# Optimization experiments

Hardware: AMD Instinct MI355X
Metric: run time of the kernel (lower is better)

The kernel has to match this reference:

```python
import jax, jax.numpy as jnp
import numpy as np

B, N, L, C, H = 4, 4096, 1024, 1024, 16
D = C // H  # head_dim = 64
SCALE = 1.0 / np.sqrt(D)


def setup_inputs() -> dict:
    key = jax.random.key(0)
    ks = jax.random.split(key, 5)
    return {
        "x": jax.random.normal(ks[0], (B, N, C), dtype=jnp.float32),
        "query": jax.random.normal(ks[1], (B, L, C), dtype=jnp.float32),
        "Wq": jax.random.normal(ks[2], (C, C), dtype=jnp.float32) * 0.02,
        "Wkv": jax.random.normal(ks[3], (2 * C, C), dtype=jnp.float32) * 0.02,
        "Wproj": jax.random.normal(ks[4], (C, C), dtype=jnp.float32) * 0.02,
        "bproj": jnp.zeros((C,), dtype=jnp.float32),
    }


def reference(x, query, Wq, Wkv, Wproj, bproj):
    # q projection: [B,L,C] -> [B,H,L,D]
    q = (query @ Wq.T).reshape(B, L, H, D).transpose(0, 2, 1, 3)
    # kv projection: [B,N,2C] -> k,v each [B,H,N,D]
    kv = (x @ Wkv.T).reshape(B, N, 2, H, D).transpose(2, 0, 3, 1, 4)
    k, v = kv[0], kv[1]
    # unfused SDPA: explicit [B,H,L,N] score matrix (faithful to source)
    attn = jnp.einsum('bhld,bhnd->bhln', q, k) * SCALE
    attn = jax.nn.softmax(attn, axis=-1)
    out = jnp.einsum('bhln,bhnd->bhld', attn, v)  # [B,H,L,D]
    out = out.transpose(0, 2, 1, 3).reshape(B, L, C)
    return out @ Wproj.T + bproj
```

## Files before the change

kernel.cpp:

```cpp
#include <hip/hip_runtime.h>
#include <hip/hip_bf16.h>

typedef __attribute__((ext_vector_type(8))) short short8;
typedef __attribute__((ext_vector_type(4))) float floatx4;

#if __has_builtin(__builtin_amdgcn_exp2f)
#define EXP2(x) __builtin_amdgcn_exp2f(x)
#else
#define EXP2(x) exp2f(x)
#endif

#define BAR() __builtin_amdgcn_s_barrier()
#define FENCE() asm volatile("" ::: "memory")
#define WAIT_LGKM0() asm volatile("s_waitcnt lgkmcnt(0)" ::: "memory")
#define WAIT_VM(n) asm volatile("s_waitcnt vmcnt(" #n ")" ::: "memory")

__device__ __forceinline__ short f2bf(float f) {
  __hip_bfloat16 h = __float2bfloat16(f);
  return *reinterpret_cast<const short*>(&h);
}

__device__ __forceinline__ short8 cvt_f32x8_bf16(const float* __restrict__ p) {
  float4 a = *reinterpret_cast<const float4*>(p);
  float4 b = *reinterpret_cast<const float4*>(p + 4);
  short8 r;
  r[0] = f2bf(a.x); r[1] = f2bf(a.y); r[2] = f2bf(a.z); r[3] = f2bf(a.w);
  r[4] = f2bf(b.x); r[5] = f2bf(b.y); r[6] = f2bf(b.z); r[7] = f2bf(b.w);
  return r;
}

typedef const __attribute__((address_space(1))) void* gptr1;
typedef __attribute__((address_space(3))) void* lptr3;
__device__ __forceinline__ void gl_lds16(const void* g, void* l) {
  __builtin_amdgcn_global_load_lds((gptr1)g, (lptr3)l, 16, 0, 0);
}

__global__ __launch_bounds__(256)
void f32_to_bf16(const float* __restrict__ in, short* __restrict__ out, int n8) {
  int i = blockIdx.x * blockDim.x + threadIdx.x;
  if (i < n8) {
    short8 v = cvt_f32x8_bf16(in + (size_t)i * 8);
    *reinterpret_cast<short8*>(out + (size_t)i * 8) = v;
  }
}

__global__ __launch_bounds__(256)
void conv_weights(const float* __restrict__ Wkv, const float* __restrict__ Wq,
                  const float* __restrict__ Wproj, short* __restrict__ wkvb,
                  short* __restrict__ wqb, short* __restrict__ wprojb) {
  const float* src; short* dst; int off;
  int i = blockIdx.x * 256 + threadIdx.x;
  if (blockIdx.x < 1024)      { src = Wkv;   dst = wkvb;   off = i; }
  else if (blockIdx.x < 1536) { src = Wq;    dst = wqb;    off = i - 1024 * 256; }
  else                        { src = Wproj; dst = wprojb; off = i - 1536 * 256; }
  short8 v = cvt_f32x8_bf16(src + (size_t)off * 8);
  *reinterpret_cast<short8*>(dst + (size_t)off * 8) = v;
}

__global__ __launch_bounds__(512, 2)
void gemm256_kv(const short* __restrict__ A, const short* __restrict__ B,
                short* __restrict__ k_out, short* __restrict__ vt,
                int M, int N, int K)
{
  __shared__ __align__(16) short lds[2][2][2][128 * 64];

  const int tid  = threadIdx.x;
  const int lane = tid & 63;
  const int w    = tid >> 6;
  const int wm   = w >> 2;
  const int wn   = w & 3;
  const int cl   = lane & 15;
  const int hi   = lane >> 4;
  const int srl  = lane >> 3;
  const int gch8 = (((lane & 7) ^ srl) << 3);

  const int ntile = N >> 8;
  int bid = blockIdx.x;
  { int cpx = gridDim.x >> 3; bid = (bid & 7) * cpx + (bid >> 3); }
  const int tm = bid / ntile, tn = bid % ntile;
  const int m0 = tm << 8, n0 = tn << 8;
  const int NT = K >> 6;

  auto stageA = [&](int par, int slot, int ktX) {
    #pragma unroll
    for (int j = 0; j < 2; ++j) {
      const int sr = (w << 4) + (j << 3) + srl;
      const int tr = ((sr >> 6) << 7) + (slot << 6) + (sr & 63);
      gl_lds16(A + (size_t)(m0 + tr) * K + ktX + gch8,
               (void*)&lds[par][0][slot][((w << 4) + (j << 3)) * 64]);
    }
  };
  auto stageB = [&](int par, int slot, int ktX) {
    #pragma unroll
    for (int j = 0; j < 2; ++j) {
      const int sr = (w << 4) + (j << 3) + srl;
      const int tr = ((sr >> 5) << 6) + (slot << 5) + (sr & 31);
      gl_lds16(B + (size_t)(n0 + tr) * K + ktX + gch8,
               (void*)&lds[par][1][slot][((w << 4) + (j << 3)) * 64]);
    }
  };

  const floatx4 fzero = {0.f, 0.f, 0.f, 0.f};
  floatx4 acc[8][4];
  #pragma unroll
  for (int m = 0; m < 8; ++m)
    #pragma unroll
    for (int n = 0; n < 4; ++n)
      acc[m][n] = fzero;

  short8 af[4][2], b0[2][2], b1[2][2];

  auto readA = [&](int par, int slot) {
    #pragma unroll
    for (int m = 0; m < 4; ++m)
      #pragma unroll
      for (int ks = 0; ks < 2; ++ks) {
        const int sr = (wm << 6) + (m << 4) + cl;
        const int cpos = ((((ks << 2) + hi) ^ (sr & 7)) << 3);
        af[m][ks] = *reinterpret_cast<const short8*>(&lds[par][0][slot][sr * 64 + cpos]);
      }
  };
  auto readB = [&](int par, int slot, short8 (&bf)[2][2]) {
    #pragma unroll
    for (int n = 0; n < 2; ++n)
      #pragma unroll
      for (int ks = 0; ks < 2; ++ks) {
        const int sr = (wn << 5) + (n << 4) + cl;
        const int cpos = ((((ks << 2) + hi) ^ (sr & 7)) << 3);
        bf[n][ks] = *reinterpret_cast<const short8*>(&lds[par][1][slot][sr * 64 + cpos]);
      }
  };

  #define QUAD(BF, MH, NH)                                                     \
    __builtin_amdgcn_s_setprio(1);                                             \
    _Pragma("unroll")                                                          \
    for (int ks = 0; ks < 2; ++ks)                                             \
      _Pragma("unroll")                                                        \
      for (int m = 0; m < 4; ++m)                                              \
        _Pragma("unroll")                                                      \
        for (int n = 0; n < 2; ++n)                                            \
          acc[(MH)*4 + m][(NH)*2 + n] = __builtin_amdgcn_mfma_f32_16x16x32_bf16( \
              af[m][ks], BF[n][ks], acc[(MH)*4 + m][(NH)*2 + n], 0, 0, 0);     \
    __builtin_amdgcn_s_setprio(0);

  stageA(0, 0, 0); stageB(0, 0, 0); stageB(0, 1, 0); stageA(0, 1, 0);
  stageA(1, 0, 64); stageB(1, 0, 64); stageB(1, 1, 64);
  WAIT_VM(6); BAR(); FENCE();

  for (int t = 0; t < NT; ++t) {
    const int p  = t & 1;
    const int pn = p ^ 1;
    int t1 = t + 1; if (t1 >= NT) t1 -= NT;
    int t2 = t + 2; if (t2 >= NT) t2 -= NT;
    const int kt1 = t1 << 6;
    const int kt2 = t2 << 6;

    readA(p, 0); readB(p, 0, b0);
    stageA(pn, 1, kt1);
    BAR(); WAIT_LGKM0();
    QUAD(b0, 0, 0);
    BAR(); FENCE();

    readB(p, 1, b1);
    stageA(p, 0, kt2);
    BAR(); WAIT_LGKM0();
    QUAD(b1, 0, 1);
    BAR(); FENCE();

    readA(p, 1);
    stageB(p, 0, kt2);
    BAR(); WAIT_LGKM0();
    QUAD(b0, 1, 0);
    BAR(); FENCE();

    stageB(p, 1, kt2);
    WAIT_VM(6);
    BAR(); WAIT_LGKM0();
    QUAD(b1, 1, 1);
    BAR(); FENCE();
  }
  WAIT_VM(0);

  const int rq = hi << 2;
  #pragma unroll
  for (int Mi = 0; Mi < 8; ++Mi) {
    #pragma unroll
    for (int Nn = 0; Nn < 4; ++Nn) {
      const int grow = m0 + wm * 128 + Mi * 16 + rq;
      const int gcol = n0 + wn * 64 + Nn * 16 + cl;
      if (gcol < 1024) {
        #pragma unroll
        for (int i = 0; i < 4; ++i)
          k_out[(size_t)(grow + i) * 1024 + gcol] = f2bf(acc[Mi][Nn][i]);
      } else {
        const int d  = gcol - 1024;
        const int bb = grow >> 12;
        const int nn = grow & 4095;
        size_t base = ((size_t)(bb * 16 + (d >> 6)) * 64 + (d & 63)) * 4096 + nn;
        short4 pk;
        pk.x = f2bf(acc[Mi][Nn][0]); pk.y = f2bf(acc[Mi][Nn][1]);
        pk.z = f2bf(acc[Mi][Nn][2]); pk.w = f2bf(acc[Mi][Nn][3]);
        *reinterpret_cast<short4*>(&vt[base]) = pk;
      }
    }
  }
}

template<int MODE>
__global__ __launch_bounds__(256, 4)
void gemm64(const short* __restrict__ A, const short* __restrict__ B,
            void* __restrict__ O0, const float* __restrict__ bias,
            int M, int N, int K, float oscale)
{
  __shared__ __align__(16) short As[64 * 64];
  __shared__ __align__(16) short Bs[64 * 64];

  const int tid  = threadIdx.x;
  const int lane = tid & 63;
  const int w    = tid >> 6;
  const int ntile = N >> 6;
  int bid = blockIdx.x;
  { int cpx = gridDim.x >> 3; bid = (bid & 7) * cpx + (bid >> 3); }
  const int tm = bid / ntile;
  const int tn = bid % ntile;
  const int m0 = tm << 6, n0 = tn << 6;
  const int wr = (w >> 1) << 5;
  const int wc = (w & 1) << 5;
  const int cl = lane & 15;
  const int hi = lane >> 4;
  const int srow = lane >> 3;
  const int scol = (lane & 7) << 3;

  const floatx4 fzero = {0.f, 0.f, 0.f, 0.f};
  floatx4 acc[2][2];
  #pragma unroll
  for (int m = 0; m < 2; ++m)
    #pragma unroll
    for (int n = 0; n < 2; ++n)
      acc[m][n] = fzero;

  for (int kt = 0; kt < K; kt += 64) {
    #pragma unroll
    for (int i = 0; i < 2; ++i) {
      const int chunk = (w << 1) + i;
      const int row   = (chunk << 3) + srow;
      gl_lds16(A + (size_t)(m0 + row) * K + kt + scol, &As[chunk * 512]);
      gl_lds16(B + (size_t)(n0 + row) * K + kt + scol, &Bs[chunk * 512]);
    }
    __syncthreads();

    #pragma unroll
    for (int ks = 0; ks < 2; ++ks) {
      short8 af[2], bfr[2];
      #pragma unroll
      for (int m = 0; m < 2; ++m)
        af[m] = *reinterpret_cast<const short8*>(
            &As[(wr + m * 16 + cl) * 64 + ks * 32 + (hi << 3)]);
      #pragma unroll
      for (int n = 0; n < 2; ++n)
        bfr[n] = *reinterpret_cast<const short8*>(
            &Bs[(wc + n * 16 + cl) * 64 + ks * 32 + (hi << 3)]);
      #pragma unroll
      for (int m = 0; m < 2; ++m)
        #pragma unroll
        for (int n = 0; n < 2; ++n)
          acc[m][n] = __builtin_amdgcn_mfma_f32_16x16x32_bf16(af[m], bfr[n], acc[m][n], 0, 0, 0);
    }
    __syncthreads();
  }

  const int rq = hi << 2;
  #pragma unroll
  for (int m = 0; m < 2; ++m) {
    #pragma unroll
    for (int n = 0; n < 2; ++n) {
      const int grow = m0 + wr + m * 16 + rq;
      const int gcol = n0 + wc + n * 16 + cl;
      if (MODE == 0) {
        short* o = (short*)O0;
        #pragma unroll
        for (int i = 0; i < 4; ++i)
          o[(size_t)(grow + i) * N + gcol] = f2bf(acc[m][n][i] * oscale);
      } else {
        float* o = (float*)O0;
        const float bv = bias[gcol];
        #pragma unroll
        for (int i = 0; i < 4; ++i)
          o[(size_t)(grow + i) * N + gcol] = acc[m][n][i] + bv;
      }
    }
  }
}

__global__ __launch_bounds__(256, 2)
void attn_fwd(const short* __restrict__ q_ws, const short* __restrict__ k_ws,
              const short* __restrict__ vt_ws, short* __restrict__ ao_ws)
{
  __shared__ __align__(16) short Ks[2][64 * 64];
  __shared__ __align__(16) short Vts[2][64 * 64];
  __shared__ __align__(16) short Pl[2][4][32 * 64];

  const int tid  = threadIdx.x;
  const int lane = tid & 63;
  const int w    = tid >> 6;
  const int i    = blockIdx.x;
  const int bh   = (i & 7) * 8 + (i >> 6);
  const int qt   = (i >> 3) & 7;
  const int b  = bh >> 4;
  const int h  = bh & 15;
  const int q0 = qt * 128 + w * 32;
  const int cl = lane & 15;
  const int hi = lane >> 4;
  const int rq = hi << 2;
  const int key7 = cl & 7;

  short8 qf[2][2];
  #pragma unroll
  for (int tt = 0; tt < 2; ++tt)
    #pragma unroll
    for (int ks = 0; ks < 2; ++ks) {
      size_t idx = (size_t)(b * 1024 + q0 + tt * 16 + cl) * 1024
                 + h * 64 + ks * 32 + (hi << 3);
      qf[tt][ks] = *reinterpret_cast<const short8*>(&q_ws[idx]);
    }

  int koff[2];
  #pragma unroll
  for (int ks = 0; ks < 2; ++ks)
    koff[ks] = cl * 64 + ((((ks << 2) + hi) ^ key7) << 3);
  const int pwc   = hi >> 1;
  const int pwoff = (hi & 1) << 2;
  int pwch[4];
  #pragma unroll
  for (int n = 0; n < 4; ++n)
    pwch[n] = ((((n << 1) + pwc) ^ key7) << 3) + pwoff + cl * 64;

  const floatx4 fzero = {0.f, 0.f, 0.f, 0.f};
  floatx4 o[2][4];
  floatx4 ol[2];
  floatx4 s[4][2];
  short8 vones;
  #pragma unroll
  for (int j = 0; j < 8; ++j) vones[j] = (short)0x3F80;
  #pragma unroll
  for (int tt = 0; tt < 2; ++tt) {
    ol[tt] = fzero;
    #pragma unroll
    for (int nd = 0; nd < 4; ++nd) o[tt][nd] = fzero;
  }

  const int c0    = w << 1;
  const int srow8 = lane >> 3;
  const int gch8  = (((lane & 7) ^ srow8) << 3);
  const short* kbase = k_ws + (size_t)(b * 4096 + (c0 << 3) + srow8) * 1024 + h * 64 + gch8;
  const short* vbase = vt_ws + ((size_t)bh * 64 + (c0 << 3) + srow8) * 4096 + gch8;

  auto stage = [&](int buf, int kv0) {
    gl_lds16(kbase + (size_t)kv0 * 1024,          (void*)&Ks[buf][c0 * 512]);
    gl_lds16(kbase + (size_t)kv0 * 1024 + 8192,   (void*)&Ks[buf][(c0 + 1) * 512]);
    gl_lds16(vbase + kv0,                          (void*)&Vts[buf][c0 * 512]);
    gl_lds16(vbase + kv0 + 8 * 4096,               (void*)&Vts[buf][(c0 + 1) * 512]);
  };

  auto qk = [&](const short* kb) {
    short8 kf[2][4];
    #pragma unroll
    for (int ks = 0; ks < 2; ++ks)
      #pragma unroll
      for (int n = 0; n < 4; ++n)
        kf[ks][n] = *reinterpret_cast<const short8*>(kb + koff[ks] + n * 1024);
    #pragma unroll
    for (int n = 0; n < 4; ++n)
      #pragma unroll
      for (int tt = 0; tt < 2; ++tt)
        s[n][tt] = __builtin_amdgcn_mfma_f32_16x16x32_bf16(
            kf[1][n], qf[tt][1],
            __builtin_amdgcn_mfma_f32_16x16x32_bf16(kf[0][n], qf[tt][0], fzero, 0, 0, 0),
            0, 0, 0);
  };
  auto pv = [&](const short* plb, const short* vb) {
    #pragma unroll
    for (int ks = 0; ks < 2; ++ks) {
      short8 pa[2], vf[4];
      #pragma unroll
      for (int tt = 0; tt < 2; ++tt)
        pa[tt] = *reinterpret_cast<const short8*>(plb + koff[ks] + tt * 1024);
      #pragma unroll
      for (int nd = 0; nd < 4; ++nd)
        vf[nd] = *reinterpret_cast<const short8*>(vb + koff[ks] + nd * 1024);
      #pragma unroll
      for (int tt = 0; tt < 2; ++tt) {
        ol[tt] = __builtin_amdgcn_mfma_f32_16x16x32_bf16(pa[tt], vones, ol[tt], 0, 0, 0);
        #pragma unroll
        for (int nd = 0; nd < 4; ++nd)
          o[tt][nd] = __builtin_amdgcn_mfma_f32_16x16x32_bf16(pa[tt], vf[nd], o[tt][nd], 0, 0, 0);
      }
    }
  };
  auto smax = [&](short* plw) {
    #pragma unroll
    for (int tt = 0; tt < 2; ++tt)
      #pragma unroll
      for (int n = 0; n < 4; ++n) {
        short4 pk;
        #pragma unroll
        for (int ii = 0; ii < 4; ++ii)
          pk[ii] = f2bf(EXP2(s[n][tt][ii]));
        *reinterpret_cast<short4*>(plw + tt * 1024 + pwch[n]) = pk;
      }
  };

  stage(0, 0);
  WAIT_VM(0); BAR(); FENCE();
  qk(&Ks[0][0]);
  stage(1, 64);
  smax(&Pl[0][w][0]);
  int pb = 0;

  for (int t = 0; t < 63; ++t) {
    const int cur = t & 1;
    WAIT_VM(0); BAR(); FENCE();
    __builtin_amdgcn_s_setprio(1);
    qk(&Ks[cur ^ 1][0]);
    pv(&Pl[pb][w][0], &Vts[cur][0]);
    __builtin_amdgcn_s_setprio(0);
    FENCE(); BAR();
    stage(cur, ((t + 2) & 63) << 6);
    smax(&Pl[pb ^ 1][w][0]);
    pb ^= 1;
  }
  __builtin_amdgcn_s_setprio(1);
  pv(&Pl[pb][w][0], &Vts[1][0]);
  __builtin_amdgcn_s_setprio(0);
  WAIT_VM(0);

  #pragma unroll
  for (int m = 0; m < 2; ++m) {
    float inv[4];
    #pragma unroll
    for (int ii = 0; ii < 4; ++ii)
      inv[ii] = 1.f / ol[m][ii];
    #pragma unroll
    for (int nd = 0; nd < 4; ++nd)
      #pragma unroll
      for (int ii = 0; ii < 4; ++ii) {
        size_t idx = (size_t)(b * 1024 + q0 + m * 16 + rq + ii) * 1024
                   + h * 64 + nd * 16 + cl;
        ao_ws[idx] = f2bf(o[m][nd][ii] * inv[ii]);
      }
  }
}

extern "C" void kernel_launch(void* const* d_in, const int* in_sizes, int n_in,
                              void* d_out, int out_size, void* d_ws, size_t ws_size,
                              hipStream_t stream)
{
  const float* x     = (const float*)d_in[0];
  const float* query = (const float*)d_in[1];
  const float* Wq    = (const float*)d_in[2];
  const float* Wkv   = (const float*)d_in[3];
  const float* Wproj = (const float*)d_in[4];
  const float* bproj = (const float*)d_in[5];
  float* out = (float*)d_out;

  const float QSCALE = 0.18033688011112042f;

  char* ws = (char*)d_ws;
  short* k_ws   = (short*)(ws);
  short* vt_ws  = (short*)(ws + (32ull << 20));
  short* xb     = (short*)(ws + (64ull << 20));
  short* qb     = (short*)(ws + (64ull << 20));
  short* q_ws   = (short*)(ws + (72ull << 20));
  short* ao_ws  = (short*)(ws + (80ull << 20));
  short* wkvb   = (short*)(ws + (96ull << 20));
  short* wqb    = (short*)(ws + (100ull << 20));
  short* wprojb = (short*)(ws + (102ull << 20));

  conv_weights<<<dim3(2048), 256, 0, stream>>>(Wkv, Wq, Wproj, wkvb, wqb, wprojb);
  f32_to_bf16<<<dim3(8192), 256, 0, stream>>>(x, xb, (16384 * 1024) / 8);

  gemm256_kv<<<dim3(512), 512, 0, stream>>>(xb, wkvb, k_ws, vt_ws,
                                            16384, 2048, 1024);
  f32_to_bf16<<<dim3(2048), 256, 0, stream>>>(query, qb, (4096 * 1024) / 8);
  gemm64<0><<<dim3(1024), 256, 0, stream>>>(qb, wqb, q_ws, nullptr,
                                            4096, 1024, 1024, QSCALE);
  attn_fwd<<<dim3(512), 256, 0, stream>>>(q_ws, k_ws, vt_ws, ao_ws);
  gemm64<2><<<dim3(1024), 256, 0, stream>>>(ao_ws, wprojb, out, bproj,
                                            4096, 1024, 1024, 1.0f);
}
```

Measured before the change: 209.8 us.

## Merge conversion kernels, fuse query cast into Q GEMM, single-buffer P in attention

Folds the x and weight fp32-to-bf16 conversions into one launch, and drops the separate query conversion by having the Q-projection GEMM read fp32 and convert while staging into LDS. The KV GEMM stops issuing wrapped-around prefetch loads on its last two iterations. The attention kernel single-buffers its P tile, adds an LDS wait before the softmax write, and raises the occupancy hint from 2 to 3 blocks per CU. The aim is fewer launches and less redundant memory traffic. The costs are synchronous register-path loads in the Q GEMM instead of direct-to-LDS copies, and less overlap in attention.

```diff
diff --git a/kernel.cpp b/kernel.cpp
--- a/kernel.cpp
+++ b/kernel.cpp
@@ -36,25 +36,19 @@
 }
 
 __global__ __launch_bounds__(256)
-void f32_to_bf16(const float* __restrict__ in, short* __restrict__ out, int n8) {
-  int i = blockIdx.x * blockDim.x + threadIdx.x;
-  if (i < n8) {
-    short8 v = cvt_f32x8_bf16(in + (size_t)i * 8);
-    *reinterpret_cast<short8*>(out + (size_t)i * 8) = v;
-  }
-}
-
-__global__ __launch_bounds__(256)
-void conv_weights(const float* __restrict__ Wkv, const float* __restrict__ Wq,
-                  const float* __restrict__ Wproj, short* __restrict__ wkvb,
-                  short* __restrict__ wqb, short* __restrict__ wprojb) {
-  const float* src; short* dst; int off;
-  int i = blockIdx.x * 256 + threadIdx.x;
-  if (blockIdx.x < 1024)      { src = Wkv;   dst = wkvb;   off = i; }
-  else if (blockIdx.x < 1536) { src = Wq;    dst = wqb;    off = i - 1024 * 256; }
-  else                        { src = Wproj; dst = wprojb; off = i - 1536 * 256; }
-  short8 v = cvt_f32x8_bf16(src + (size_t)off * 8);
-  *reinterpret_cast<short8*>(dst + (size_t)off * 8) = v;
+void conv_all(const float* __restrict__ x, const float* __restrict__ Wkv,
+              const float* __restrict__ Wq, const float* __restrict__ Wproj,
+              short* __restrict__ xb, short* __restrict__ wkvb,
+              short* __restrict__ wqb, short* __restrict__ wprojb) {
+  const float* src; short* dst; size_t off;
+  int bi = blockIdx.x;
+  int i = bi * 256 + threadIdx.x;
+  if (bi < 8192)      { src = x;     dst = xb;     off = i; }
+  else if (bi < 9216) { src = Wkv;   dst = wkvb;   off = i - 8192 * 256; }
+  else if (bi < 9728) { src = Wq;    dst = wqb;    off = i - 9216 * 256; }
+  else                { src = Wproj; dst = wprojb; off = i - 9728 * 256; }
+  short8 v = cvt_f32x8_bf16(src + off * 8);
+  *reinterpret_cast<short8*>(dst + off * 8) = v;
 }
 
 __global__ __launch_bounds__(512, 2)
@@ -150,36 +144,35 @@
   for (int t = 0; t < NT; ++t) {
     const int p  = t & 1;
     const int pn = p ^ 1;
-    int t1 = t + 1; if (t1 >= NT) t1 -= NT;
-    int t2 = t + 2; if (t2 >= NT) t2 -= NT;
+    const int t1 = t + 1;
+    const int t2 = t + 2;
     const int kt1 = t1 << 6;
     const int kt2 = t2 << 6;
 
     readA(p, 0); readB(p, 0, b0);
-    stageA(pn, 1, kt1);
+    if (t1 < NT) stageA(pn, 1, kt1);
     BAR(); WAIT_LGKM0();
     QUAD(b0, 0, 0);
     BAR(); FENCE();
 
     readB(p, 1, b1);
-    stageA(p, 0, kt2);
+    if (t2 < NT) stageA(p, 0, kt2);
     BAR(); WAIT_LGKM0();
     QUAD(b1, 0, 1);
     BAR(); FENCE();
 
     readA(p, 1);
-    stageB(p, 0, kt2);
+    if (t2 < NT) stageB(p, 0, kt2);
     BAR(); WAIT_LGKM0();
     QUAD(b0, 1, 0);
     BAR(); FENCE();
 
-    stageB(p, 1, kt2);
-    WAIT_VM(6);
+    if (t2 < NT) { stageB(p, 1, kt2); WAIT_VM(6); }
+    else         { WAIT_VM(0); }
     BAR(); WAIT_LGKM0();
     QUAD(b1, 1, 1);
     BAR(); FENCE();
   }
-  WAIT_VM(0);
 
   const int rq = hi << 2;
   #pragma unroll
@@ -206,9 +199,9 @@
   }
 }
 
-template<int MODE>
+template<int MODE, bool AFP32>
 __global__ __launch_bounds__(256, 4)
-void gemm64(const short* __restrict__ A, const short* __restrict__ B,
+void gemm64(const void* __restrict__ Ap, const short* __restrict__ B,
             void* __restrict__ O0, const float* __restrict__ bias,
             int M, int N, int K, float oscale)
 {
@@ -240,11 +233,29 @@
       acc[m][n] = fzero;
 
   for (int kt = 0; kt < K; kt += 64) {
+    if (AFP32) {
+      const float* A = (const float*)Ap;
+      #pragma unroll
+      for (int sgm = 0; sgm < 2; ++sgm) {
+        const int seg = tid + sgm * 256;
+        const int row = seg >> 3;
+        const int c8  = (seg & 7) << 3;
+        short8 v = cvt_f32x8_bf16(A + (size_t)(m0 + row) * K + kt + c8);
+        *reinterpret_cast<short8*>(&As[row * 64 + c8]) = v;
+      }
+    } else {
+      const short* A = (const short*)Ap;
+      #pragma unroll
+      for (int i = 0; i < 2; ++i) {
+        const int chunk = (w << 1) + i;
+        const int row   = (chunk << 3) + srow;
+        gl_lds16(A + (size_t)(m0 + row) * K + kt + scol, &As[chunk * 512]);
+      }
+    }
     #pragma unroll
     for (int i = 0; i < 2; ++i) {
       const int chunk = (w << 1) + i;
       const int row   = (chunk << 3) + srow;
-      gl_lds16(A + (size_t)(m0 + row) * K + kt + scol, &As[chunk * 512]);
       gl_lds16(B + (size_t)(n0 + row) * K + kt + scol, &Bs[chunk * 512]);
     }
     __syncthreads();
@@ -292,13 +303,13 @@
   }
 }
 
-__global__ __launch_bounds__(256, 2)
+__global__ __launch_bounds__(256, 3)
 void attn_fwd(const short* __restrict__ q_ws, const short* __restrict__ k_ws,
               const short* __restrict__ vt_ws, short* __restrict__ ao_ws)
 {
   __shared__ __align__(16) short Ks[2][64 * 64];
   __shared__ __align__(16) short Vts[2][64 * 64];
-  __shared__ __align__(16) short Pl[2][4][32 * 64];
+  __shared__ __align__(16) short Pl[4][32 * 64];
 
   const int tid  = threadIdx.x;
   const int lane = tid & 63;
@@ -414,23 +425,22 @@
   WAIT_VM(0); BAR(); FENCE();
   qk(&Ks[0][0]);
   stage(1, 64);
-  smax(&Pl[0][w][0]);
-  int pb = 0;
+  smax(&Pl[w][0]);
 
   for (int t = 0; t < 63; ++t) {
     const int cur = t & 1;
     WAIT_VM(0); BAR(); FENCE();
     __builtin_amdgcn_s_setprio(1);
     qk(&Ks[cur ^ 1][0]);
-    pv(&Pl[pb][w][0], &Vts[cur][0]);
+    pv(&Pl[w][0], &Vts[cur][0]);
     __builtin_amdgcn_s_setprio(0);
     FENCE(); BAR();
     stage(cur, ((t + 2) & 63) << 6);
-    smax(&Pl[pb ^ 1][w][0]);
-    pb ^= 1;
+    WAIT_LGKM0();
+    smax(&Pl[w][0]);
   }
   __builtin_amdgcn_s_setprio(1);
-  pv(&Pl[pb][w][0], &Vts[1][0]);
+  pv(&Pl[w][0], &Vts[1][0]);
   __builtin_amdgcn_s_setprio(0);
   WAIT_VM(0);
 
@@ -469,22 +479,19 @@
   short* k_ws   = (short*)(ws);
   short* vt_ws  = (short*)(ws + (32ull << 20));
   short* xb     = (short*)(ws + (64ull << 20));
-  short* qb     = (short*)(ws + (64ull << 20));
   short* q_ws   = (short*)(ws + (72ull << 20));
   short* ao_ws  = (short*)(ws + (80ull << 20));
   short* wkvb   = (short*)(ws + (96ull << 20));
   short* wqb    = (short*)(ws + (100ull << 20));
   short* wprojb = (short*)(ws + (102ull << 20));
 
-  conv_weights<<<dim3(2048), 256, 0, stream>>>(Wkv, Wq, Wproj, wkvb, wqb, wprojb);
-  f32_to_bf16<<<dim3(8192), 256, 0, stream>>>(x, xb, (16384 * 1024) / 8);
-
+  conv_all<<<dim3(10240), 256, 0, stream>>>(x, Wkv, Wq, Wproj,
+                                            xb, wkvb, wqb, wprojb);
   gemm256_kv<<<dim3(512), 512, 0, stream>>>(xb, wkvb, k_ws, vt_ws,
                                             16384, 2048, 1024);
-  f32_to_bf16<<<dim3(2048), 256, 0, stream>>>(query, qb, (4096 * 1024) / 8);
-  gemm64<0><<<dim3(1024), 256, 0, stream>>>(qb, wqb, q_ws, nullptr,
-                                            4096, 1024, 1024, QSCALE);
+  gemm64<0, true><<<dim3(1024), 256, 0, stream>>>(query, wqb, q_ws, nullptr,
+                                                  4096, 1024, 1024, QSCALE);
   attn_fwd<<<dim3(512), 256, 0, stream>>>(q_ws, k_ws, vt_ws, ao_ws);
-  gemm64<2><<<dim3(1024), 256, 0, stream>>>(ao_ws, wprojb, out, bproj,
-                                            4096, 1024, 1024, 1.0f);
-}
+  gemm64<2, false><<<dim3(1024), 256, 0, stream>>>(ao_ws, wprojb, out, bproj,
+                                                   4096, 1024, 1024, 1.0f);
+}
```

Result: slower. 214.6 us (+2.3%).
